# Kernel optimization log

Measured on AMD Instinct MI355X. Metric: run time of the kernel, lower is better.

Reference implementation:

```python
import jax, jax.numpy as jnp
import numpy as np

B, S, D = 2, 2048, 1024
H, HD = 16, 64          # num_heads, head_dim = D // H
W = 31                  # window_size (odd)
E = 1024                # embed_dim


def setup_inputs() -> dict:
    key = jax.random.key(0)
    ks = jax.random.split(key, 12)
    sd = 1.0 / np.sqrt(D)
    so = 1.0 / np.sqrt(H * HD)
    return {
        "x": jax.random.normal(ks[0], (B, S, D), jnp.float32),
        "fsq": jax.random.normal(ks[1], (1, S, D), jnp.float32),   # feature_squeeze_token
        "pos": jax.random.normal(ks[2], (1, S, D), jnp.float32),   # position_token
        "Wq": jax.random.normal(ks[3], (H, D, HD), jnp.float32) * sd,
        "bq": jax.random.normal(ks[4], (H, HD), jnp.float32) * sd,
        "Wk": jax.random.normal(ks[5], (H, D, HD), jnp.float32) * sd,
        "bk": jax.random.normal(ks[6], (H, HD), jnp.float32) * sd,
        "Wv": jax.random.normal(ks[7], (H, D, HD), jnp.float32) * sd,
        "bv": jax.random.normal(ks[8], (H, HD), jnp.float32) * sd,
        "Wo": jax.random.normal(ks[9], (H * HD, E), jnp.float32) * so,
        "bo": jax.random.normal(ks[10], (E,), jnp.float32) * so,
    }


def reference(x, fsq, pos, Wq, bq, Wk, bk, Wv, bv, Wo, bo):
    b, s, d = x.shape
    pad = (W - 1) // 2
    # sliding windows: (B, S, W, D), zero-padded at sequence edges
    xp = jnp.pad(x, ((0, 0), (pad, pad), (0, 0)))
    idx = jnp.arange(s)[:, None] + jnp.arange(W)[None, :]  # (S, W)
    win = xp[:, idx, :]  # (B, S, W, D)
    a = jnp.broadcast_to(fsq[:, :, None, :], (b, s, 1, d))  # squeeze token per pos
    bt = jnp.broadcast_to(pos[:, :, None, :], (b, s, 1, d))  # position token per pos
    kv = jnp.concatenate([win, bt, a], axis=2)  # (B, S, K=W+2, D)
    q = jnp.broadcast_to(fsq, (b, s, d))        # query = squeeze token
    # per-head projections (heads stacked on axis h)
    qh = jnp.einsum("bsd,hde->bhse", q, Wq) + bq[None, :, None, :]        # (B,H,S,HD)
    kh = jnp.einsum("bskd,hde->bhske", kv, Wk) + bk[None, :, None, None, :]
    vh = jnp.einsum("bskd,hde->bhske", kv, Wv) + bv[None, :, None, None, :]
    scores = jnp.einsum("bhse,bhske->bhsk", qh, kh) / jnp.sqrt(jnp.asarray(HD, x.dtype))
    attn = jax.nn.softmax(scores, axis=-1)  # dropout is identity in eval
    outh = jnp.einsum("bhsk,bhske->bhse", attn, vh)  # (B,H,S,HD)
    concat = outh.transpose(0, 2, 1, 3).reshape(b, s, H * HD)  # heads concat order 0..H-1
    return concat @ Wo + bo  # (B, S, E)
```

## Files before the change

kernel.cpp:

```cpp
#include <hip/hip_runtime.h>


typedef __attribute__((ext_vector_type(8))) short bf16x8;
typedef __attribute__((ext_vector_type(4))) float f32x4;
typedef unsigned short u16;
typedef unsigned int u32;
typedef unsigned long long u64;

__device__ __forceinline__ float bf2f(u16 u) {
  union { u32 i; float f; } v; v.i = ((u32)u) << 16; return v.f;
}
__device__ __forceinline__ u16 f2bf(float f) {
  union { float f; u32 i; } v; v.f = f;
  u32 r = v.i + 0x7fffu + ((v.i >> 16) & 1u);
  return (u16)(r >> 16);
}
__device__ __forceinline__ float2 unpk(u32 u) {
  union { u32 i; float f; } lo, hi;
  lo.i = u << 16; hi.i = u & 0xffff0000u;
  return make_float2(lo.f, hi.f);
}
__device__ __forceinline__ float dot8(uint4 a, uint4 b) {
  float s = 0.f;
  { float2 x = unpk(a.x), y = unpk(b.x); s += x.x*y.x + x.y*y.y; }
  { float2 x = unpk(a.y), y = unpk(b.y); s += x.x*y.x + x.y*y.y; }
  { float2 x = unpk(a.z), y = unpk(b.z); s += x.x*y.x + x.y*y.y; }
  { float2 x = unpk(a.w), y = unpk(b.w); s += x.x*y.x + x.y*y.y; }
  return s;
}
__device__ __forceinline__ void gload_lds16(const u16* g, u16* l) {
  __builtin_amdgcn_global_load_lds((const __attribute__((address_space(1))) void*)(g),
                                   (__attribute__((address_space(3))) void*)(l),
                                   16, 0, 0);
}
__device__ __forceinline__ uint4 pack8(float4 a, float4 b) {
  union { u16 h[8]; uint4 q; } u;
  u.h[0] = f2bf(a.x); u.h[1] = f2bf(a.y); u.h[2] = f2bf(a.z); u.h[3] = f2bf(a.w);
  u.h[4] = f2bf(b.x); u.h[5] = f2bf(b.y); u.h[6] = f2bf(b.z); u.h[7] = f2bf(b.w);
  return u.q;
}

__device__ __forceinline__ void transpose_body(const float* src, u16* dst,
                                               int R, int C, int r0, int c0) {
  __shared__ u16 tile[64][72];
  int t = threadIdx.x;
#pragma unroll
  for (int i = 0; i < 16; ++i) {
    int idx = i * 256 + t;
    int r = idx >> 6, c = idx & 63;
    tile[r][c] = f2bf(src[(size_t)(r0 + r) * C + (c0 + c)]);
  }
  __syncthreads();
#pragma unroll
  for (int i = 0; i < 16; ++i) {
    int idx = i * 256 + t;
    int c = idx >> 6, r = idx & 63;
    dst[(size_t)(c0 + c) * R + (r0 + r)] = tile[r][c];
  }
}

__global__ __launch_bounds__(256) void prep(const float* __restrict__ x,
                                            const float* __restrict__ fsq,
                                            const float* __restrict__ pos,
                                            const float* __restrict__ Wq,
                                            const float* __restrict__ Wk,
                                            const float* __restrict__ Wv,
                                            const float* __restrict__ Wo,
                                            u16* __restrict__ xb,
                                            u16* __restrict__ fsqb,
                                            u16* __restrict__ posb,
                                            u16* __restrict__ WqT,
                                            u16* __restrict__ WkT,
                                            u16* __restrict__ WvT,
                                            u16* __restrict__ WoT) {
  int bid = blockIdx.x;
  if (bid < 4096) {
    int i = bid * 256 + threadIdx.x;
    const float* src; u16* dst; int off;
    if (i < 524288)      { src = x;   dst = xb;   off = i; }
    else if (i < 786432) { src = fsq; dst = fsqb; off = i - 524288; }
    else                 { src = pos; dst = posb; off = i - 786432; }
    float4 a = ((const float4*)src)[2 * off];
    float4 b = ((const float4*)src)[2 * off + 1];
    ((uint4*)dst)[off] = pack8(a, b);
  } else {
    int id = bid - 4096;
    int z = id >> 8, rest = id & 255;
    int xx = rest & 15, yy = rest >> 4;
    if (z < 3) {
      const float* s = (z == 0) ? Wq : (z == 1) ? Wk : Wv;
      u16* d = (z == 0) ? WqT : (z == 1) ? WkT : WvT;
      size_t off = (size_t)xx * 65536;
      transpose_body(s + off, d + off, 1024, 64, yy * 64, 0);
    } else {
      transpose_body(Wo, WoT, 1024, 1024, yy * 64, xx * 64);
    }
  }
}

__device__ __forceinline__ int swz(int R, int c) {
  return (R * 8 + (c ^ (R & 7))) * 8;
}

template <int MT, int OMODE>
__device__ __forceinline__ void gemm_body(u16* __restrict__ As,
                                          u16* __restrict__ Bs,
                                          const u16* __restrict__ Ap,
                                          const u16* __restrict__ BT,
                                          const float* __restrict__ bias,
                                          void* Cp, int tile_n, int tile_m) {
  const int t = threadIdx.x, lane = t & 63, wave = t >> 6;
  const int wm = (wave >> 1) * (MT * 16), wn = (wave & 1) * 64;
  const int row16 = lane & 15, quad = lane >> 4;
  const int l8 = lane >> 3;
  const int cswz = (lane & 7) ^ l8;

  f32x4 acc[MT][4] = {};

  for (int k0 = 0; k0 < 1024; k0 += 64) {
    __syncthreads();
#pragma unroll
    for (int j = 0; j < MT; ++j) {
      int r = wave * (MT * 8) + j * 8 + l8;
      gload_lds16(Ap + (size_t)r * 1024 + k0 + cswz * 8,
                  &As[wave * (MT * 512) + j * 512]);
    }
#pragma unroll
    for (int j = 0; j < 4; ++j) {
      int r = wave * 32 + j * 8 + l8;
      gload_lds16(BT + (size_t)(tile_n + r) * 1024 + k0 + cswz * 8,
                  &Bs[wave * 2048 + j * 512]);
    }
    __syncthreads();

#pragma unroll
    for (int kb = 0; kb < 2; ++kb) {
      bf16x8 a_frag[MT], b_frag[4];
#pragma unroll
      for (int i = 0; i < MT; ++i)
        a_frag[i] = *(const bf16x8*)&As[swz(wm + i * 16 + row16, kb * 4 + quad)];
#pragma unroll
      for (int j = 0; j < 4; ++j)
        b_frag[j] = *(const bf16x8*)&Bs[swz(wn + j * 16 + row16, kb * 4 + quad)];
#pragma unroll
      for (int i = 0; i < MT; ++i)
#pragma unroll
        for (int j = 0; j < 4; ++j)
          acc[i][j] = __builtin_amdgcn_mfma_f32_16x16x32_bf16(
              a_frag[i], b_frag[j], acc[i][j], 0, 0, 0);
    }
  }

#pragma unroll
  for (int j = 0; j < 4; ++j) {
    int n = tile_n + wn + j * 16 + row16;
    float bb = bias[n];
#pragma unroll
    for (int i = 0; i < MT; ++i) {
      int m0 = wm + i * 16 + quad * 4;
      if (OMODE == 2) {
        union { u16 h[4]; u64 q; } o;
#pragma unroll
        for (int r = 0; r < 4; ++r) o.h[r] = f2bf(acc[i][j][r] + bb);
        *(u64*)((u16*)Cp + (size_t)n * 4096 + tile_m + m0) = o.q;
      } else {
#pragma unroll
        for (int r = 0; r < 4; ++r) {
          float val = acc[i][j][r] + bb;
          if (OMODE == 1) ((float*)Cp)[(size_t)(m0 + r) * 1024 + n] = val;
          else            ((u16*)Cp)[(size_t)(m0 + r) * 1024 + n] = f2bf(val);
        }
      }
    }
  }
}

__global__ __launch_bounds__(256) void proj_gemm(const u16* __restrict__ xb,
                                                 const u16* __restrict__ fsqb,
                                                 const u16* __restrict__ posb,
                                                 const u16* __restrict__ WkT,
                                                 const u16* __restrict__ WvT,
                                                 const u16* __restrict__ WqT,
                                                 const float* __restrict__ bk,
                                                 const float* __restrict__ bv,
                                                 const float* __restrict__ bq,
                                                 u16* __restrict__ Kp,
                                                 u16* __restrict__ VpT,
                                                 u16* __restrict__ Vd,
                                                 u16* __restrict__ Qp) {
  __shared__ u16 As[128 * 64];
  __shared__ u16 Bs[128 * 64];
  int bid = blockIdx.x;
  if (bid < 1024) {
    int tm = bid >> 4, tn = bid & 15;
    const u16* Ap;
    if (tm < 32)      Ap = xb   + (size_t)tm * 128 * 1024;
    else if (tm < 48) Ap = fsqb + (size_t)(tm - 32) * 128 * 1024;
    else              Ap = posb + (size_t)(tm - 48) * 128 * 1024;
    if (tn < 8) {
      gemm_body<4, 0>(As, Bs, Ap, WkT, bk,
                      Kp + (size_t)tm * 128 * 1024, tn * 128, 0);
    } else if (tm < 32) {
      gemm_body<4, 2>(As, Bs, Ap, WvT, bv, VpT, (tn - 8) * 128, tm * 128);
    } else {
      gemm_body<4, 0>(As, Bs, Ap, WvT, bv,
                      Vd + (size_t)(tm - 32) * 128 * 1024, (tn - 8) * 128, 0);
    }
  } else {
    int qb = bid - 1024;
    int tm = qb >> 3, tn = qb & 7;
    gemm_body<4, 0>(As, Bs, fsqb + (size_t)tm * 128 * 1024, WqT, bq,
                    Qp + (size_t)tm * 128 * 1024, tn * 128, 0);
  }
}

__global__ __launch_bounds__(256) void out_gemm(const u16* __restrict__ Att,
                                                const u16* __restrict__ WoT,
                                                const float* __restrict__ bo,
                                                float* __restrict__ Out) {
  __shared__ u16 As[64 * 64];
  __shared__ u16 Bs[128 * 64];
  int tile_n = blockIdx.x * 128, tm = blockIdx.y;
  gemm_body<2, 1>(As, Bs, Att + (size_t)tm * 64 * 1024, WoT, bo,
                  Out + (size_t)tm * 64 * 1024, tile_n, 0);
}

#define QS   0
#define KPS  2304
#define KFS  4608
#define KWS  6912
#define VTS  11008
#define SMT  15104

__global__ __launch_bounds__(256) void attn_tile(const u16* __restrict__ Qp,
                                                 const u16* __restrict__ Kp,
                                                 const u16* __restrict__ VpT,
                                                 const u16* __restrict__ Vd,
                                                 const float* __restrict__ bk,
                                                 const float* __restrict__ bv,
                                                 u16* __restrict__ Att) {
  __shared__ u16 sm[SMT];
  __shared__ float smP[32 * 36];

  const int t = threadIdx.x;
  const int bid = blockIdx.x;
  const int s0 = (bid & 63) * 32;
  const int h  = (bid >> 6) & 15;
  const int b  = bid >> 10;
  const int lane = t & 63, wave = t >> 6;
  const int row16 = lane & 15, quad = lane >> 4;
  const int hcol = h * 64;

  { int w = t >> 3, oct = t & 7;
    *(uint4*)&sm[QS + w * 72 + oct * 8] =
        *(const uint4*)(Qp + (size_t)(s0 + w) * 1024 + hcol + oct * 8); }
  { int r = t >> 3, oct = t & 7;
    *(uint4*)&sm[KPS + r * 72 + oct * 8] =
        *(const uint4*)(Kp + (size_t)(6144 + s0 + r) * 1024 + hcol + oct * 8);
    *(uint4*)&sm[KFS + r * 72 + oct * 8] =
        *(const uint4*)(Kp + (size_t)(4096 + s0 + r) * 1024 + hcol + oct * 8); }

  const bool boundary = (s0 == 0) || (s0 == 2016);
  if (!boundary) {
#pragma unroll
    for (int i = 0; i < 2; ++i) {
      int task = i * 256 + t;
      int w = task >> 3, oct = task & 7;
      gload_lds16(Kp + (size_t)(b * 2048 + s0 + w - 16) * 1024 + hcol + oct * 8,
                  &sm[KWS + (i * 256 + wave * 64) * 8]);
      int e = w;
      gload_lds16(VpT + (size_t)(hcol + e) * 4096 + (b * 2048 + s0 - 16) + oct * 8,
                  &sm[VTS + (i * 256 + wave * 64) * 8]);
    }
  } else {
#pragma unroll
    for (int i = 0; i < 2; ++i) {
      int task = i * 256 + t;
      int w = task >> 3, oct = task & 7;
      int g = s0 + w - 16;
      uint4 kv;
      if ((unsigned)g < 2048u)
        kv = *(const uint4*)(Kp + (size_t)(b * 2048 + g) * 1024 + hcol + oct * 8);
      else
        kv = pack8(*(const float4*)(bk + hcol + oct * 8),
                   *(const float4*)(bk + hcol + oct * 8 + 4));
      *(uint4*)&sm[KWS + w * 64 + oct * 8] = kv;

      int e = w;
      int g0 = s0 + oct * 8 - 16;
      uint4 vv;
      if (g0 >= 0 && g0 + 7 < 2048)
        vv = *(const uint4*)(VpT + (size_t)(hcol + e) * 4096 + (b * 2048 + g0));
      else {
        u16 hb = f2bf(bv[hcol + e]);
        u32 pp = (u32)hb | ((u32)hb << 16);
        vv = make_uint4(pp, pp, pp, pp);
      }
      *(uint4*)&sm[VTS + e * 64 + oct * 8] = vv;
    }
  }
  __syncthreads();

  {
    f32x4 accS[2] = {};
#pragma unroll
    for (int kc = 0; kc < 2; ++kc) {
      bf16x8 bf_ = *(const bf16x8*)&sm[KWS + (wave * 16 + row16) * 64 + kc * 32 + quad * 8];
#pragma unroll
      for (int mi = 0; mi < 2; ++mi) {
        bf16x8 af = *(const bf16x8*)&sm[QS + (mi * 16 + row16) * 72 + kc * 32 + quad * 8];
        accS[mi] = __builtin_amdgcn_mfma_f32_16x16x32_bf16(af, bf_, accS[mi], 0, 0, 0);
      }
    }
#pragma unroll
    for (int mi = 0; mi < 2; ++mi)
#pragma unroll
      for (int r = 0; r < 4; ++r) {
        int s = mi * 16 + quad * 4 + r;
        int w = wave * 16 + row16;
        int d = w - s;
        if (d >= 1 && d <= 31) smP[s * 36 + d - 1] = accS[mi][r] * 0.125f;
      }
  }
  if (t < 64) {
    int s = t >> 1, which = t & 1;
    int base = (which == 0) ? KPS : KFS;
    float a = 0.f;
#pragma unroll
    for (int c = 0; c < 8; ++c)
      a += dot8(*(const uint4*)&sm[QS + s * 72 + c * 8],
                *(const uint4*)&sm[base + s * 72 + c * 8]);
    smP[s * 36 + 31 + which] = a * 0.125f;
  }
  __syncthreads();

  if (t < 32) {
    int s = t;
    float vals[33];
#pragma unroll
    for (int k = 0; k < 33; ++k) vals[k] = smP[s * 36 + k];
    float mx = -1e30f;
#pragma unroll
    for (int k = 0; k < 33; ++k) mx = fmaxf(mx, vals[k]);
    float sum = 0.f;
#pragma unroll
    for (int k = 0; k < 33; ++k) { vals[k] = __expf(vals[k] - mx); sum += vals[k]; }
    float inv = 1.f / sum;
    u32* prow = (u32*)&sm[QS + s * 72];
#pragma unroll
    for (int j = 0; j < 32; ++j) prow[j] = 0;
#pragma unroll
    for (int k = 0; k < 31; ++k)
      sm[QS + s * 72 + (s + 1 + k)] = f2bf(vals[k] * inv);
    smP[s * 36 + 33] = vals[31] * inv;
    smP[s * 36 + 34] = vals[32] * inv;
  }
  __syncthreads();

  {
    f32x4 accO[2] = {};
#pragma unroll
    for (int kc = 0; kc < 2; ++kc) {
      bf16x8 bf_ = *(const bf16x8*)&sm[VTS + (wave * 16 + row16) * 64 + kc * 32 + quad * 8];
#pragma unroll
      for (int mi = 0; mi < 2; ++mi) {
        bf16x8 af = *(const bf16x8*)&sm[QS + (mi * 16 + row16) * 72 + kc * 32 + quad * 8];
        accO[mi] = __builtin_amdgcn_mfma_f32_16x16x32_bf16(af, bf_, accO[mi], 0, 0, 0);
      }
    }
#pragma unroll
    for (int mi = 0; mi < 2; ++mi)
#pragma unroll
      for (int r = 0; r < 4; ++r) {
        int s = mi * 16 + quad * 4 + r;
        int e = wave * 16 + row16;
        float o = accO[mi][r]
                + smP[s * 36 + 33] * bf2f(Vd[(size_t)(2048 + s0 + s) * 1024 + hcol + e])
                + smP[s * 36 + 34] * bf2f(Vd[(size_t)(s0 + s) * 1024 + hcol + e]);
        Att[(size_t)(b * 2048 + s0 + s) * 1024 + hcol + e] = f2bf(o);
      }
  }
}

extern "C" void kernel_launch(void* const* d_in, const int* in_sizes, int n_in,
                              void* d_out, int out_size, void* d_ws, size_t ws_size,
                              hipStream_t stream) {
  (void)in_sizes; (void)n_in; (void)out_size; (void)ws_size;

  const float* x   = (const float*)d_in[0];
  const float* fsq = (const float*)d_in[1];
  const float* pos = (const float*)d_in[2];
  const float* Wq  = (const float*)d_in[3];
  const float* bq  = (const float*)d_in[4];
  const float* Wk  = (const float*)d_in[5];
  const float* bk  = (const float*)d_in[6];
  const float* Wv  = (const float*)d_in[7];
  const float* bv  = (const float*)d_in[8];
  const float* Wo  = (const float*)d_in[9];
  const float* bo  = (const float*)d_in[10];

  u16* ws = (u16*)d_ws;
  const size_t M1 = 1024 * 1024;
  u16* WqT  = ws + 0 * M1;
  u16* WkT  = ws + 1 * M1;
  u16* WvT  = ws + 2 * M1;
  u16* WoT  = ws + 3 * M1;
  u16* Qp   = ws + 4 * M1;
  u16* Kp   = ws + 6 * M1;
  u16* VpT  = ws + 14 * M1;
  u16* Vd   = ws + 18 * M1;
  u16* fsqb = ws + 22 * M1;
  u16* posb = ws + 24 * M1;
  u16* xb   = ws + 26 * M1;
  u16* Att  = ws + 22 * M1;

  prep<<<5120, 256, 0, stream>>>(x, fsq, pos, Wq, Wk, Wv, Wo,
                                 xb, fsqb, posb, WqT, WkT, WvT, WoT);

  proj_gemm<<<1152, 256, 0, stream>>>(xb, fsqb, posb, WkT, WvT, WqT,
                                      bk, bv, bq, Kp, VpT, Vd, Qp);

  attn_tile<<<2048, 256, 0, stream>>>(Qp, Kp, VpT, Vd, bk, bv, Att);

  out_gemm<<<dim3(8, 64), 256, 0, stream>>>(Att, WoT, bo, (float*)d_out);
}
```

Before: 197.1 us.

## Widen projection GEMM tiles to 128x256 so K and V share A loads

The projection GEMM now uses 512-thread blocks computing 128x256 output tiles. Each block pairs the K and V weight slices (or two Q slices), so every A tile is loaded into LDS once and used for both outputs. This halves the block count and the redundant activation loads. In exchange each block needs more LDS and registers, and with only 576 blocks occupancy and load balance across CUs may drop. The out GEMM is just inlined from the removed template with no behavioural change.

```diff
diff --git a/kernel.cpp b/kernel.cpp
--- a/kernel.cpp
+++ b/kernel.cpp
@@ -102,80 +102,7 @@
   return (R * 8 + (c ^ (R & 7))) * 8;
 }
 
-template <int MT, int OMODE>
-__device__ __forceinline__ void gemm_body(u16* __restrict__ As,
-                                          u16* __restrict__ Bs,
-                                          const u16* __restrict__ Ap,
-                                          const u16* __restrict__ BT,
-                                          const float* __restrict__ bias,
-                                          void* Cp, int tile_n, int tile_m) {
-  const int t = threadIdx.x, lane = t & 63, wave = t >> 6;
-  const int wm = (wave >> 1) * (MT * 16), wn = (wave & 1) * 64;
-  const int row16 = lane & 15, quad = lane >> 4;
-  const int l8 = lane >> 3;
-  const int cswz = (lane & 7) ^ l8;
-
-  f32x4 acc[MT][4] = {};
-
-  for (int k0 = 0; k0 < 1024; k0 += 64) {
-    __syncthreads();
-#pragma unroll
-    for (int j = 0; j < MT; ++j) {
-      int r = wave * (MT * 8) + j * 8 + l8;
-      gload_lds16(Ap + (size_t)r * 1024 + k0 + cswz * 8,
-                  &As[wave * (MT * 512) + j * 512]);
-    }
-#pragma unroll
-    for (int j = 0; j < 4; ++j) {
-      int r = wave * 32 + j * 8 + l8;
-      gload_lds16(BT + (size_t)(tile_n + r) * 1024 + k0 + cswz * 8,
-                  &Bs[wave * 2048 + j * 512]);
-    }
-    __syncthreads();
-
-#pragma unroll
-    for (int kb = 0; kb < 2; ++kb) {
-      bf16x8 a_frag[MT], b_frag[4];
-#pragma unroll
-      for (int i = 0; i < MT; ++i)
-        a_frag[i] = *(const bf16x8*)&As[swz(wm + i * 16 + row16, kb * 4 + quad)];
-#pragma unroll
-      for (int j = 0; j < 4; ++j)
-        b_frag[j] = *(const bf16x8*)&Bs[swz(wn + j * 16 + row16, kb * 4 + quad)];
-#pragma unroll
-      for (int i = 0; i < MT; ++i)
-#pragma unroll
-        for (int j = 0; j < 4; ++j)
-          acc[i][j] = __builtin_amdgcn_mfma_f32_16x16x32_bf16(
-              a_frag[i], b_frag[j], acc[i][j], 0, 0, 0);
-    }
-  }
-
-#pragma unroll
-  for (int j = 0; j < 4; ++j) {
-    int n = tile_n + wn + j * 16 + row16;
-    float bb = bias[n];
-#pragma unroll
-    for (int i = 0; i < MT; ++i) {
-      int m0 = wm + i * 16 + quad * 4;
-      if (OMODE == 2) {
-        union { u16 h[4]; u64 q; } o;
-#pragma unroll
-        for (int r = 0; r < 4; ++r) o.h[r] = f2bf(acc[i][j][r] + bb);
-        *(u64*)((u16*)Cp + (size_t)n * 4096 + tile_m + m0) = o.q;
-      } else {
-#pragma unroll
-        for (int r = 0; r < 4; ++r) {
-          float val = acc[i][j][r] + bb;
-          if (OMODE == 1) ((float*)Cp)[(size_t)(m0 + r) * 1024 + n] = val;
-          else            ((u16*)Cp)[(size_t)(m0 + r) * 1024 + n] = f2bf(val);
-        }
-      }
-    }
-  }
-}
-
-__global__ __launch_bounds__(256) void proj_gemm(const u16* __restrict__ xb,
+__global__ __launch_bounds__(512) void proj_gemm(const u16* __restrict__ xb,
                                                  const u16* __restrict__ fsqb,
                                                  const u16* __restrict__ posb,
                                                  const u16* __restrict__ WkT,
@@ -189,28 +116,123 @@
                                                  u16* __restrict__ Vd,
                                                  u16* __restrict__ Qp) {
   __shared__ u16 As[128 * 64];
-  __shared__ u16 Bs[128 * 64];
-  int bid = blockIdx.x;
-  if (bid < 1024) {
-    int tm = bid >> 4, tn = bid & 15;
-    const u16* Ap;
-    if (tm < 32)      Ap = xb   + (size_t)tm * 128 * 1024;
-    else if (tm < 48) Ap = fsqb + (size_t)(tm - 32) * 128 * 1024;
-    else              Ap = posb + (size_t)(tm - 48) * 128 * 1024;
-    if (tn < 8) {
-      gemm_body<4, 0>(As, Bs, Ap, WkT, bk,
-                      Kp + (size_t)tm * 128 * 1024, tn * 128, 0);
-    } else if (tm < 32) {
-      gemm_body<4, 2>(As, Bs, Ap, WvT, bv, VpT, (tn - 8) * 128, tm * 128);
-    } else {
-      gemm_body<4, 0>(As, Bs, Ap, WvT, bv,
-                      Vd + (size_t)(tm - 32) * 128 * 1024, (tn - 8) * 128, 0);
-    }
+  __shared__ u16 Bs[256 * 64];
+
+  const int bid = blockIdx.x;
+  const int t = threadIdx.x, lane = t & 63, wave = t >> 6;
+  const int row16 = lane & 15, quad = lane >> 4;
+  const int l8 = lane >> 3;
+  const int cswz = (lane & 7) ^ l8;
+
+  const u16 *Ap, *BTa, *BTb;
+  const float *biasA, *biasB;
+  u16 *C1, *C2rm;
+  int c1_noff, c2_noff;
+  bool c2_t = false;
+  int tmb = 0;
+
+  if (bid < 512) {
+    int tm = bid >> 3, tn = bid & 7;
+    if (tm < 32)      Ap = xb   + (size_t)tm * 131072;
+    else if (tm < 48) Ap = fsqb + (size_t)(tm - 32) * 131072;
+    else              Ap = posb + (size_t)(tm - 48) * 131072;
+    BTa = WkT + (size_t)(tn * 128) * 1024;
+    BTb = WvT + (size_t)(tn * 128) * 1024;
+    biasA = bk; biasB = bv;
+    C1 = Kp + (size_t)tm * 131072; c1_noff = tn * 128;
+    c2_noff = tn * 128;
+    if (tm < 32) { c2_t = true; tmb = tm * 128; C2rm = nullptr; }
+    else         { C2rm = Vd + (size_t)(tm - 32) * 131072; }
   } else {
-    int qb = bid - 1024;
-    int tm = qb >> 3, tn = qb & 7;
-    gemm_body<4, 0>(As, Bs, fsqb + (size_t)tm * 128 * 1024, WqT, bq,
-                    Qp + (size_t)tm * 128 * 1024, tn * 128, 0);
+    int q = bid - 512;
+    int tm = q >> 2, tn4 = q & 3;
+    Ap  = fsqb + (size_t)tm * 131072;
+    BTa = WqT + (size_t)(tn4 * 256) * 1024;
+    BTb = WqT + (size_t)(tn4 * 256 + 128) * 1024;
+    biasA = bq; biasB = bq;
+    C1 = Qp + (size_t)tm * 131072;  c1_noff = tn4 * 256;
+    C2rm = C1;                      c2_noff = tn4 * 256 + 128;
+  }
+
+  const int wm = (wave >> 2) * 64, wn = (wave & 3) * 64;
+  f32x4 acc[4][4] = {};
+
+  for (int k0 = 0; k0 < 1024; k0 += 64) {
+    __syncthreads();
+#pragma unroll
+    for (int j = 0; j < 2; ++j) {
+      int r = wave * 16 + j * 8 + l8;
+      gload_lds16(Ap + (size_t)r * 1024 + k0 + cswz * 8,
+                  &As[wave * 1024 + j * 512]);
+    }
+    const u16* Bsrc = (wave < 4) ? BTa : BTb;
+    const int rb = (wave & 3) * 32;
+#pragma unroll
+    for (int j = 0; j < 4; ++j) {
+      int r = rb + j * 8 + l8;
+      gload_lds16(Bsrc + (size_t)r * 1024 + k0 + cswz * 8,
+                  &Bs[wave * 2048 + j * 512]);
+    }
+    __syncthreads();
+
+#pragma unroll
+    for (int kb = 0; kb < 2; ++kb) {
+      bf16x8 a_frag[4], b_frag[4];
+#pragma unroll
+      for (int i = 0; i < 4; ++i)
+        a_frag[i] = *(const bf16x8*)&As[swz(wm + i * 16 + row16, kb * 4 + quad)];
+#pragma unroll
+      for (int j = 0; j < 4; ++j)
+        b_frag[j] = *(const bf16x8*)&Bs[swz(wn + j * 16 + row16, kb * 4 + quad)];
+#pragma unroll
+      for (int i = 0; i < 4; ++i)
+#pragma unroll
+        for (int j = 0; j < 4; ++j)
+          acc[i][j] = __builtin_amdgcn_mfma_f32_16x16x32_bf16(
+              a_frag[i], b_frag[j], acc[i][j], 0, 0, 0);
+    }
+  }
+
+  if (wn < 128) {
+#pragma unroll
+    for (int j = 0; j < 4; ++j) {
+      int n = c1_noff + wn + j * 16 + row16;
+      float bb = biasA[n];
+#pragma unroll
+      for (int i = 0; i < 4; ++i) {
+        int m0 = wm + i * 16 + quad * 4;
+#pragma unroll
+        for (int r = 0; r < 4; ++r)
+          C1[(size_t)(m0 + r) * 1024 + n] = f2bf(acc[i][j][r] + bb);
+      }
+    }
+  } else if (c2_t) {
+#pragma unroll
+    for (int j = 0; j < 4; ++j) {
+      int nv = c2_noff + (wn - 128) + j * 16 + row16;
+      float bb = biasB[nv];
+#pragma unroll
+      for (int i = 0; i < 4; ++i) {
+        int m0 = wm + i * 16 + quad * 4;
+        union { u16 h[4]; u64 q; } o;
+#pragma unroll
+        for (int r = 0; r < 4; ++r) o.h[r] = f2bf(acc[i][j][r] + bb);
+        *(u64*)(VpT + (size_t)nv * 4096 + tmb + m0) = o.q;
+      }
+    }
+  } else {
+#pragma unroll
+    for (int j = 0; j < 4; ++j) {
+      int nv = c2_noff + (wn - 128) + j * 16 + row16;
+      float bb = biasB[nv];
+#pragma unroll
+      for (int i = 0; i < 4; ++i) {
+        int m0 = wm + i * 16 + quad * 4;
+#pragma unroll
+        for (int r = 0; r < 4; ++r)
+          C2rm[(size_t)(m0 + r) * 1024 + nv] = f2bf(acc[i][j][r] + bb);
+      }
+    }
   }
 }
 
@@ -220,9 +242,64 @@
                                                 float* __restrict__ Out) {
   __shared__ u16 As[64 * 64];
   __shared__ u16 Bs[128 * 64];
-  int tile_n = blockIdx.x * 128, tm = blockIdx.y;
-  gemm_body<2, 1>(As, Bs, Att + (size_t)tm * 64 * 1024, WoT, bo,
-                  Out + (size_t)tm * 64 * 1024, tile_n, 0);
+  const int tile_n = blockIdx.x * 128, tm = blockIdx.y;
+  const u16* Ap = Att + (size_t)tm * 65536;
+  float* Cp = Out + (size_t)tm * 65536;
+
+  const int t = threadIdx.x, lane = t & 63, wave = t >> 6;
+  const int wm = (wave >> 1) * 32, wn = (wave & 1) * 64;
+  const int row16 = lane & 15, quad = lane >> 4;
+  const int l8 = lane >> 3;
+  const int cswz = (lane & 7) ^ l8;
+
+  f32x4 acc[2][4] = {};
+
+  for (int k0 = 0; k0 < 1024; k0 += 64) {
+    __syncthreads();
+#pragma unroll
+    for (int j = 0; j < 2; ++j) {
+      int r = wave * 16 + j * 8 + l8;
+      gload_lds16(Ap + (size_t)r * 1024 + k0 + cswz * 8,
+                  &As[wave * 1024 + j * 512]);
+    }
+#pragma unroll
+    for (int j = 0; j < 4; ++j) {
+      int r = wave * 32 + j * 8 + l8;
+      gload_lds16(WoT + (size_t)(tile_n + r) * 1024 + k0 + cswz * 8,
+                  &Bs[wave * 2048 + j * 512]);
+    }
+    __syncthreads();
+
+#pragma unroll
+    for (int kb = 0; kb < 2; ++kb) {
+      bf16x8 a_frag[2], b_frag[4];
+#pragma unroll
+      for (int i = 0; i < 2; ++i)
+        a_frag[i] = *(const bf16x8*)&As[swz(wm + i * 16 + row16, kb * 4 + quad)];
+#pragma unroll
+      for (int j = 0; j < 4; ++j)
+        b_frag[j] = *(const bf16x8*)&Bs[swz(wn + j * 16 + row16, kb * 4 + quad)];
+#pragma unroll
+      for (int i = 0; i < 2; ++i)
+#pragma unroll
+        for (int j = 0; j < 4; ++j)
+          acc[i][j] = __builtin_amdgcn_mfma_f32_16x16x32_bf16(
+              a_frag[i], b_frag[j], acc[i][j], 0, 0, 0);
+    }
+  }
+
+#pragma unroll
+  for (int j = 0; j < 4; ++j) {
+    int n = tile_n + wn + j * 16 + row16;
+    float bb = bo[n];
+#pragma unroll
+    for (int i = 0; i < 2; ++i) {
+      int m0 = wm + i * 16 + quad * 4;
+#pragma unroll
+      for (int r = 0; r < 4; ++r)
+        Cp[(size_t)(m0 + r) * 1024 + n] = acc[i][j][r] + bb;
+    }
+  }
 }
 
 #define QS   0
@@ -417,8 +494,8 @@
   prep<<<5120, 256, 0, stream>>>(x, fsq, pos, Wq, Wk, Wv, Wo,
                                  xb, fsqb, posb, WqT, WkT, WvT, WoT);
 
-  proj_gemm<<<1152, 256, 0, stream>>>(xb, fsqb, posb, WkT, WvT, WqT,
-                                      bk, bv, bq, Kp, VpT, Vd, Qp);
+  proj_gemm<<<576, 512, 0, stream>>>(xb, fsqb, posb, WkT, WvT, WqT,
+                                     bk, bv, bq, Kp, VpT, Vd, Qp);
 
   attn_tile<<<2048, 256, 0, stream>>>(Qp, Kp, VpT, Vd, bk, bv, Att);
 
```

Result: slower. 201.4 us (+2.2%).
